# Performance work log

Measured on AMD Instinct MI355X. Metric: run time of the kernel, lower is better.

The kernel has to match this reference:

```python
import jax, jax.numpy as jnp
import numpy as np

NUM_HEADS = 16
N_EMBED = 1024
HEAD_SIZE = 64
BLOCK_SIZE = 2048


def setup_inputs() -> dict:
    key = jax.random.key(0)
    ks = jax.random.split(key, 6)
    B, S, C, H, D = 2, BLOCK_SIZE, N_EMBED, NUM_HEADS, HEAD_SIZE
    x = jax.random.normal(ks[0], (B, S, C), dtype=jnp.float32)
    scale = C ** -0.5
    # per-head q/k/v projections (bias=False), stacked over heads: [H, C, D]
    Wq = jax.random.normal(ks[1], (H, C, D), dtype=jnp.float32) * scale
    Wk = jax.random.normal(ks[2], (H, C, D), dtype=jnp.float32) * scale
    Wv = jax.random.normal(ks[3], (H, C, D), dtype=jnp.float32) * scale
    # output projection Linear(H*D, C)
    Wo = jax.random.normal(ks[4], (H * D, C), dtype=jnp.float32) * ((H * D) ** -0.5)
    bo = jax.random.normal(ks[5], (C,), dtype=jnp.float32) * 0.01
    return {"x": x, "Wq": Wq, "Wk": Wk, "Wv": Wv, "Wo": Wo, "bo": bo}


def reference(x, Wq, Wk, Wv, Wo, bo):
    B, S, C = x.shape
    H, _, D = Wq.shape
    # project: [B, H, S, D]
    q = jnp.einsum("bsc,hcd->bhsd", x, Wq)
    k = jnp.einsum("bsc,hcd->bhsd", x, Wk)
    v = jnp.einsum("bsc,hcd->bhsd", x, Wv)
    # scaled causal attention scores: [B, H, S, S]
    scores = jnp.einsum("bhsd,bhtd->bhst", q, k) * (D ** -0.5)
    causal = jnp.tril(jnp.ones((S, S), dtype=bool))
    scores = jnp.where(causal, scores, jnp.finfo(scores.dtype).min)
    attn = jax.nn.softmax(scores, axis=-1)
    out = jnp.einsum("bhst,bhtd->bhsd", attn, v)  # [B, H, S, D]
    # concat heads -> [B, S, H*D], then output projection
    out = out.transpose(0, 2, 1, 3).reshape(B, S, H * D)
    return out @ Wo + bo
```

## Files before the change

kernel.cpp:

```cpp
#include <hip/hip_runtime.h>
#include <cstdint>
#include <cstddef>

constexpr int SEQ  = 2048;
constexpr int CH   = 1024;
constexpr int NH   = 16;
constexpr int HS   = 64;
constexpr int NB   = 2;
constexpr int HDIM = NH * HS;

typedef __bf16 bf16x8 __attribute__((ext_vector_type(8)));
typedef __bf16 bf16x4 __attribute__((ext_vector_type(4)));
typedef float  f32x4  __attribute__((ext_vector_type(4)));

__device__ __forceinline__ unsigned short f2bf(float f) {
  union { float f; unsigned u; } v; v.f = f;
  unsigned u = v.u;
  u += 0x7fffu + ((u >> 16) & 1u);
  return (unsigned short)(u >> 16);
}
__device__ __forceinline__ float bf2f(unsigned short h) {
  union { unsigned u; float f; } v; v.u = ((unsigned)h) << 16;
  return v.f;
}
__device__ __forceinline__ float load_elem(const void* p, int flag, size_t idx) {
  if (flag) return ((const float*)p)[idx];
  return bf2f(((const unsigned short*)p)[idx]);
}
__device__ __forceinline__ void gl_lds16(const unsigned short* g, unsigned short* l) {
  __builtin_amdgcn_global_load_lds(
      (const __attribute__((address_space(1))) unsigned int*)g,
      (__attribute__((address_space(3))) unsigned int*)l, 16, 0, 0);
}

__device__ int detect_flag_block(const void* p, int n, int tid, int nthr) {
  __shared__ int det_good;
  if (tid == 0) det_good = 0;
  __syncthreads();
  const unsigned short* u = (const unsigned short*)p;
  int good = 0;
  for (int j = tid; j < n; j += nthr) {
    unsigned short v = u[2 * j];
    int e = (v >> 7) & 0xFF;
    if (v != 0 && e >= 90 && e <= 150) good++;
  }
  atomicAdd(&det_good, good);
  __syncthreads();
  return (det_good * 10 >= n * 7) ? 0 : 1;
}

__global__ __launch_bounds__(256) void prep(
    const void* __restrict__ x,  const void* __restrict__ wq,
    const void* __restrict__ wk, const void* __restrict__ wv,
    const void* __restrict__ wo,
    unsigned short* __restrict__ xb,
    unsigned short* __restrict__ wall,
    unsigned short* __restrict__ wot) {
  __shared__ unsigned short tile[32][36];
  int idx = blockIdx.x, tid = threadIdx.x;
  int row = tid >> 3, cg = (tid & 7) * 4;
  int col = tid >> 3, rg = (tid & 7) * 4;
  if (idx < 1024) {
    int f = detect_flag_block(x, 512, tid, 256);
    size_t n4 = (size_t)NB * SEQ * CH / 4;
    for (size_t i = (size_t)idx * 256 + tid; i < n4; i += (size_t)1024 * 256) {
      ushort4 o;
      if (f) {
        float4 v = ((const float4*)x)[i];
        o.x = f2bf(v.x); o.y = f2bf(v.y); o.z = f2bf(v.z); o.w = f2bf(v.w);
      } else {
        o = ((const ushort4*)x)[i];
      }
      ((ushort4*)xb)[i] = o;
    }
  } else if (idx < 4096) {
    int j = idx - 1024;
    int which = j >> 10, hh = (j >> 6) & 15, sub = j & 63;
    const void* src = (which == 0) ? wq : (which == 1) ? wk : wv;
    int f = detect_flag_block(src, 512, tid, 256);
    int c0 = (sub & 1) * 32;
    int r0 = (sub >> 1) * 32;
    size_t boff = (size_t)hh * CH * HS;
    size_t si = boff + (size_t)(r0 + row) * HS + c0 + cg;
    ushort4 t4;
    if (f) {
      float4 v = *(const float4*)((const float*)src + si);
      t4.x = f2bf(v.x); t4.y = f2bf(v.y); t4.z = f2bf(v.z); t4.w = f2bf(v.w);
    } else {
      t4 = *(const ushort4*)((const unsigned short*)src + si);
    }
    *(ushort4*)&tile[row][cg] = t4;
    __syncthreads();
    unsigned short* d = wall + ((size_t)which * NH + hh) * HS * CH;
    ushort4 o;
    o.x = tile[rg + 0][col]; o.y = tile[rg + 1][col];
    o.z = tile[rg + 2][col]; o.w = tile[rg + 3][col];
    *(ushort4*)&d[(size_t)(c0 + col) * CH + r0 + rg] = o;
  } else {
    int sub = idx - 4096;
    int f = detect_flag_block(wo, 512, tid, 256);
    int c0 = (sub & 31) * 32;
    int r0 = (sub >> 5) * 32;
    size_t si = (size_t)(r0 + row) * CH + c0 + cg;
    ushort4 t4;
    if (f) {
      float4 v = *(const float4*)((const float*)wo + si);
      t4.x = f2bf(v.x); t4.y = f2bf(v.y); t4.z = f2bf(v.z); t4.w = f2bf(v.w);
    } else {
      t4 = *(const ushort4*)((const unsigned short*)wo + si);
    }
    *(ushort4*)&tile[row][cg] = t4;
    __syncthreads();
    ushort4 o;
    o.x = tile[rg + 0][col]; o.y = tile[rg + 1][col];
    o.z = tile[rg + 2][col]; o.w = tile[rg + 3][col];
    *(ushort4*)&wot[(size_t)(c0 + col) * HDIM + r0 + rg] = o;
  }
}

__global__ __launch_bounds__(256, 2) void qkv_gemm(
    const unsigned short* __restrict__ xb,
    const unsigned short* __restrict__ wall,
    unsigned short* __restrict__ qo,
    unsigned short* __restrict__ ko,
    unsigned short* __restrict__ vt) {
  __shared__ __attribute__((aligned(16))) unsigned short Al[2][128 * 64];
  __shared__ __attribute__((aligned(16))) unsigned short Bl[2][192 * 64];
  int mt = blockIdx.x, nt = blockIdx.y;
  const unsigned short* A  = xb   + (size_t)mt * 128 * CH;
  const unsigned short* Bm = wall + (size_t)nt * 192 * CH;
  int tid = threadIdx.x, wave = tid >> 6, lane = tid & 63;
  int quad = lane >> 4, l15 = lane & 15;
  int r8 = lane >> 3, c8 = lane & 7;
  int gcol = ((c8 ^ r8) << 3);
  int x7 = l15 & 7;
  int wm = (wave >> 1) * 64, wn = (wave & 1) * 96;
  f32x4 acc[4][6];
  #pragma unroll
  for (int i = 0; i < 4; i++)
    #pragma unroll
    for (int j = 0; j < 6; j++) acc[i][j] = (f32x4){0.f, 0.f, 0.f, 0.f};

  auto stage = [&](int bb, int k0) {
    #pragma unroll
    for (int c = 0; c < 4; c++) {
      int row = wave * 32 + c * 8 + r8;
      gl_lds16(&A[(size_t)row * CH + k0 + gcol], &Al[bb][(wave * 32 + c * 8) * 64]);
    }
    #pragma unroll
    for (int c = 0; c < 6; c++) {
      int row = wave * 48 + c * 8 + r8;
      gl_lds16(&Bm[(size_t)row * CH + k0 + gcol], &Bl[bb][(wave * 48 + c * 8) * 64]);
    }
  };

  stage(0, 0);
  __syncthreads();
  for (int ks = 0; ks < 16; ks++) {
    int bb = ks & 1;
    if (ks < 15) stage(bb ^ 1, (ks + 1) * 64);
    #pragma unroll
    for (int h = 0; h < 2; h++) {
      int cq = ((quad + 4 * h) ^ x7) << 3;
      bf16x8 af[4], bfr[6];
      #pragma unroll
      for (int fm = 0; fm < 4; fm++)
        af[fm] = *reinterpret_cast<const bf16x8*>(&Al[bb][(wm + fm * 16 + l15) * 64 + cq]);
      #pragma unroll
      for (int fn = 0; fn < 6; fn++)
        bfr[fn] = *reinterpret_cast<const bf16x8*>(&Bl[bb][(wn + fn * 16 + l15) * 64 + cq]);
      __builtin_amdgcn_s_setprio(1);
      #pragma unroll
      for (int fm = 0; fm < 4; fm++)
        #pragma unroll
        for (int fn = 0; fn < 6; fn++)
          acc[fm][fn] = __builtin_amdgcn_mfma_f32_16x16x32_bf16(af[fm], bfr[fn], acc[fm][fn], 0, 0, 0);
      __builtin_amdgcn_s_setprio(0);
    }
    __syncthreads();
  }

  #pragma unroll
  for (int fn = 0; fn < 6; fn++) {
    int c0 = nt * 192 + wn + fn * 16;
    int seg = c0 >> 10;
    int hd = (c0 & 1023) + l15;
    int h = hd >> 6, d = hd & 63;
    if (seg < 2) {
      unsigned short* dst = (seg == 0) ? qo : ko;
      float s = (seg == 0) ? 0.18033688011112042f : 1.0f;
      #pragma unroll
      for (int fm = 0; fm < 4; fm++) {
        int m = mt * 128 + wm + fm * 16 + quad * 4;
        int b = m >> 11, s0 = m & 2047;
        #pragma unroll
        for (int r = 0; r < 4; r++)
          dst[(((size_t)b * NH + h) * SEQ + s0 + r) * HS + d] = f2bf(acc[fm][fn][r] * s);
      }
    } else {
      #pragma unroll
      for (int fm = 0; fm < 4; fm++) {
        int m = mt * 128 + wm + fm * 16 + quad * 4;
        int b = m >> 11, s0 = m & 2047;
        ushort4 pk;
        pk.x = f2bf(acc[fm][fn][0]); pk.y = f2bf(acc[fm][fn][1]);
        pk.z = f2bf(acc[fm][fn][2]); pk.w = f2bf(acc[fm][fn][3]);
        *(ushort4*)&vt[(((size_t)b * NH + h) * HS + d) * SEQ + s0] = pk;
      }
    }
  }
}

template <bool MASKED>
__device__ __forceinline__ void soft_pack(const f32x4* s, f32x4& ls,
                                          unsigned short* ptRow, int quad, int tmb) {
  #pragma unroll
  for (int tb = 0; tb < 4; tb++) {
    f32x4 pv;
    #pragma unroll
    for (int r = 0; r < 4; r++) {
      float p = __builtin_amdgcn_exp2f(s[tb][r]);
      if (MASKED) { if (tmb + tb * 16 + quad * 4 + r > 0) p = 0.f; }
      pv[r] = p;
    }
    ls += pv;
    bf16x4 pk;
    pk.x = (__bf16)pv[0]; pk.y = (__bf16)pv[1];
    pk.z = (__bf16)pv[2]; pk.w = (__bf16)pv[3];
    *(bf16x4*)&ptRow[tb * 16 + quad * 4] = pk;
  }
}

template <int QKM, bool PV0, bool PVV>
__device__ __forceinline__ void attn_step(
    const unsigned short (&Kb)[64][64], const unsigned short (&Vp)[64][64],
    unsigned short* p0row, unsigned short* p1row,
    const bf16x8 (&qf)[2][2], f32x4 (&lsum)[2], f32x4 (&accO)[2][4],
    int quad, int l15, int tmb) {
  constexpr bool C0 = (QKM <= 1);
  constexpr bool M0 = (QKM == 1);
  constexpr bool M1 = (QKM == 3);
  int x7 = l15 & 7;
  bf16x8 pb0[2], pb1[2];
  if (PVV) {
    #pragma unroll
    for (int tp = 0; tp < 2; tp++) {
      if (PV0) pb0[tp] = *reinterpret_cast<const bf16x8*>(&p0row[tp * 32 + quad * 8]);
      pb1[tp] = *reinterpret_cast<const bf16x8*>(&p1row[tp * 32 + quad * 8]);
    }
  }
  f32x4 s0[4], s1[4];
  #pragma unroll
  for (int tb = 0; tb < 4; tb++) { s0[tb] = (f32x4){0,0,0,0}; s1[tb] = (f32x4){0,0,0,0}; }
  __builtin_amdgcn_s_setprio(1);
  #pragma unroll
  for (int tb = 0; tb < 4; tb++)
    #pragma unroll
    for (int hh = 0; hh < 2; hh++) {
      bf16x8 kf = *reinterpret_cast<const bf16x8*>(
          &Kb[tb * 16 + l15][((hh * 4 + quad) ^ x7) << 3]);
      if (C0) s0[tb] = __builtin_amdgcn_mfma_f32_16x16x32_bf16(kf, qf[0][hh], s0[tb], 0, 0, 0);
      s1[tb] = __builtin_amdgcn_mfma_f32_16x16x32_bf16(kf, qf[1][hh], s1[tb], 0, 0, 0);
    }
  if (PVV) {
    #pragma unroll
    for (int db = 0; db < 4; db++)
      #pragma unroll
      for (int tp = 0; tp < 2; tp++) {
        bf16x8 vf = *reinterpret_cast<const bf16x8*>(
            &Vp[db * 16 + l15][((tp * 4 + quad) ^ x7) << 3]);
        if (PV0) accO[0][db] = __builtin_amdgcn_mfma_f32_16x16x32_bf16(vf, pb0[tp], accO[0][db], 0, 0, 0);
        accO[1][db] = __builtin_amdgcn_mfma_f32_16x16x32_bf16(vf, pb1[tp], accO[1][db], 0, 0, 0);
      }
  }
  __builtin_amdgcn_s_setprio(0);
  if (C0) soft_pack<M0>(s0, lsum[0], p0row, quad, tmb);
  soft_pack<M1>(s1, lsum[1], p1row, quad, tmb);
}

__global__ __launch_bounds__(256) void attn_k(
    const unsigned short* __restrict__ q,
    const unsigned short* __restrict__ k,
    const unsigned short* __restrict__ vt,
    unsigned short* __restrict__ y) {
  __shared__ __attribute__((aligned(16))) unsigned short Kl[3][64][64];
  __shared__ __attribute__((aligned(16))) unsigned short Vl[3][64][64];
  __shared__ __attribute__((aligned(16))) unsigned short Pt[4][16][152];

  int n = blockIdx.x + 16 * blockIdx.y;
  int g = n & 7, idx = n >> 3;
  int p = idx & 15;
  int bh = g * 4 + (idx >> 4);
  int st0 = p, st1 = 31 - p;
  int b = bh >> 4, h = bh & 15;
  const unsigned short* Q0 = q + ((size_t)bh * SEQ + st0 * 64) * HS;
  const unsigned short* Q1 = q + ((size_t)bh * SEQ + st1 * 64) * HS;
  const unsigned short* K  = k  + (size_t)bh * SEQ * HS;
  const unsigned short* V  = vt + (size_t)bh * HS * SEQ;
  int tid = threadIdx.x, wave = tid >> 6, lane = tid & 63;
  int quad = lane >> 4, l15 = lane & 15;
  int lr = tid >> 3, lc = (tid & 7) * 8;
  int sc = (((tid & 7) ^ (lr & 7)) << 3);

  bf16x8 qf[2][2];
  #pragma unroll
  for (int hh = 0; hh < 2; hh++) {
    qf[0][hh] = *reinterpret_cast<const bf16x8*>(
        &Q0[(size_t)(wave * 16 + l15) * HS + hh * 32 + quad * 8]);
    qf[1][hh] = *reinterpret_cast<const bf16x8*>(
        &Q1[(size_t)(wave * 16 + l15) * HS + hh * 32 + quad * 8]);
  }

  f32x4 lsum[2] = {(f32x4){0,0,0,0}, (f32x4){0,0,0,0}};
  f32x4 accO[2][4];
  #pragma unroll
  for (int f = 0; f < 2; f++)
    #pragma unroll
    for (int i = 0; i < 4; i++) accO[f][i] = (f32x4){0.f, 0.f, 0.f, 0.f};

  unsigned short* p0row = &Pt[wave][l15][0];
  unsigned short* p1row = &Pt[wave][l15][64];
  int tmb = -(wave * 16 + l15);

  const unsigned short* pK0 = K + (size_t)lr * HS + lc;
  const unsigned short* pK1 = pK0 + (size_t)32 * HS;
  const unsigned short* pV0 = V + (size_t)lr * SEQ + lc;
  const unsigned short* pV1 = pV0 + (size_t)32 * SEQ;
  uint4 kr0, kr1, vr0, vr1;
  auto g2r = [&]() {
    kr0 = *(const uint4*)pK0; kr1 = *(const uint4*)pK1;
    vr0 = *(const uint4*)pV0; vr1 = *(const uint4*)pV1;
    pK0 += 64 * HS; pK1 += 64 * HS; pV0 += 64; pV1 += 64;
  };
  auto r2l = [&](int nb) {
    *(uint4*)&Kl[nb][lr][sc] = kr0; *(uint4*)&Kl[nb][lr + 32][sc] = kr1;
    *(uint4*)&Vl[nb][lr][sc] = vr0; *(uint4*)&Vl[nb][lr + 32][sc] = vr1;
  };

  g2r(); r2l(0);
  __syncthreads();

  {
    if (st1 > 0) g2r();
    if (st0 == 0)
      attn_step<1, false, false>(Kl[0], Vl[2], p0row, p1row, qf, lsum, accO, quad, l15, tmb);
    else
      attn_step<0, false, false>(Kl[0], Vl[2], p0row, p1row, qf, lsum, accO, quad, l15, tmb);
    if (st1 > 0) r2l(1);
    __syncthreads();
  }
  for (int t = 1; t < st0; t++) {
    g2r();
    attn_step<0, true, true>(Kl[t % 3], Vl[(t + 2) % 3], p0row, p1row, qf, lsum, accO, quad, l15, tmb);
    r2l((t + 1) % 3);
    __syncthreads();
  }
  if (st0 >= 1) {
    int t = st0;
    g2r();
    attn_step<1, true, true>(Kl[t % 3], Vl[(t + 2) % 3], p0row, p1row, qf, lsum, accO, quad, l15, tmb);
    r2l((t + 1) % 3);
    __syncthreads();
  }
  {
    int t = st0 + 1;
    bool more = (t < st1);
    if (more) g2r();
    if (t == st1)
      attn_step<3, true, true>(Kl[t % 3], Vl[(t + 2) % 3], p0row, p1row, qf, lsum, accO, quad, l15, tmb);
    else
      attn_step<2, true, true>(Kl[t % 3], Vl[(t + 2) % 3], p0row, p1row, qf, lsum, accO, quad, l15, tmb);
    if (more) r2l((t + 1) % 3);
    __syncthreads();
  }
  for (int t = st0 + 2; t < st1; t++) {
    g2r();
    attn_step<2, false, true>(Kl[t % 3], Vl[(t + 2) % 3], p0row, p1row, qf, lsum, accO, quad, l15, tmb);
    r2l((t + 1) % 3);
    __syncthreads();
  }
  if (st1 >= st0 + 2) {
    int t = st1;
    attn_step<3, false, true>(Kl[t % 3], Vl[(t + 2) % 3], p0row, p1row, qf, lsum, accO, quad, l15, tmb);
  }
  {
    const unsigned short (&Vb)[64][64] = Vl[st1 % 3];
    int x7 = l15 & 7;
    bf16x8 pb1[2];
    #pragma unroll
    for (int tp = 0; tp < 2; tp++)
      pb1[tp] = *reinterpret_cast<const bf16x8*>(&p1row[tp * 32 + quad * 8]);
    #pragma unroll
    for (int db = 0; db < 4; db++)
      #pragma unroll
      for (int tp = 0; tp < 2; tp++) {
        bf16x8 vf = *reinterpret_cast<const bf16x8*>(
            &Vb[db * 16 + l15][((tp * 4 + quad) ^ x7) << 3]);
        accO[1][db] = __builtin_amdgcn_mfma_f32_16x16x32_bf16(vf, pb1[tp], accO[1][db], 0, 0, 0);
      }
  }

  #pragma unroll
  for (int f = 0; f < 2; f++) {
    float rs = (lsum[f][0] + lsum[f][1]) + (lsum[f][2] + lsum[f][3]);
    rs += __shfl_xor(rs, 16); rs += __shfl_xor(rs, 32);
    float inv = 1.0f / fmaxf(rs, 1e-30f);
    int srow = (f == 0 ? st0 : st1) * 64 + wave * 16 + l15;
    #pragma unroll
    for (int db = 0; db < 4; db++) {
      ushort4 pk;
      pk.x = f2bf(accO[f][db][0] * inv); pk.y = f2bf(accO[f][db][1] * inv);
      pk.z = f2bf(accO[f][db][2] * inv); pk.w = f2bf(accO[f][db][3] * inv);
      *(ushort4*)&y[((size_t)b * SEQ + srow) * HDIM + h * 64 + db * 16 + quad * 4] = pk;
    }
  }
}

__global__ __launch_bounds__(256) void out_gemm(
    const unsigned short* __restrict__ y,
    const unsigned short* __restrict__ wot,
    const void* __restrict__ bo,
    float* __restrict__ out) {
  __shared__ __attribute__((aligned(16))) unsigned short Al[2][128 * 64];
  __shared__ __attribute__((aligned(16))) unsigned short Bl[2][64 * 64];
  int tid = threadIdx.x;
  int fbo = detect_flag_block(bo, 512, tid, 256);
  int mt = blockIdx.x, nt = blockIdx.y;
  const unsigned short* A  = y   + (size_t)mt * 128 * HDIM;
  const unsigned short* Bm = wot + (size_t)nt * 64 * HDIM;
  int wave = tid >> 6, lane = tid & 63;
  int quad = lane >> 4, l15 = lane & 15;
  int r8 = lane >> 3, c8 = lane & 7;
  int gcol = ((c8 ^ r8) << 3);
  int x7 = l15 & 7;
  int wm = (wave >> 1) * 64, wn = (wave & 1) * 32;
  f32x4 acc[4][2];
  #pragma unroll
  for (int i = 0; i < 4; i++)
    #pragma unroll
    for (int j = 0; j < 2; j++) acc[i][j] = (f32x4){0.f, 0.f, 0.f, 0.f};

  auto stage = [&](int bb, int k0) {
    #pragma unroll
    for (int c = 0; c < 4; c++) {
      int row = wave * 32 + c * 8 + r8;
      gl_lds16(&A[(size_t)row * HDIM + k0 + gcol], &Al[bb][(wave * 32 + c * 8) * 64]);
    }
    #pragma unroll
    for (int c = 0; c < 2; c++) {
      int row = wave * 16 + c * 8 + r8;
      gl_lds16(&Bm[(size_t)row * HDIM + k0 + gcol], &Bl[bb][(wave * 16 + c * 8) * 64]);
    }
  };

  stage(0, 0);
  __syncthreads();
  for (int ks = 0; ks < 16; ks++) {
    int bb = ks & 1;
    if (ks < 15) stage(bb ^ 1, (ks + 1) * 64);
    #pragma unroll
    for (int h = 0; h < 2; h++) {
      int cq = ((quad + 4 * h) ^ x7) << 3;
      bf16x8 af[4], bfr[2];
      #pragma unroll
      for (int fm = 0; fm < 4; fm++)
        af[fm] = *reinterpret_cast<const bf16x8*>(&Al[bb][(wm + fm * 16 + l15) * 64 + cq]);
      #pragma unroll
      for (int fn = 0; fn < 2; fn++)
        bfr[fn] = *reinterpret_cast<const bf16x8*>(&Bl[bb][(wn + fn * 16 + l15) * 64 + cq]);
      __builtin_amdgcn_s_setprio(1);
      #pragma unroll
      for (int fm = 0; fm < 4; fm++)
        #pragma unroll
        for (int fn = 0; fn < 2; fn++)
          acc[fm][fn] = __builtin_amdgcn_mfma_f32_16x16x32_bf16(af[fm], bfr[fn], acc[fm][fn], 0, 0, 0);
      __builtin_amdgcn_s_setprio(0);
    }
    __syncthreads();
  }

  #pragma unroll
  for (int fn = 0; fn < 2; fn++) {
    int n = nt * 64 + wn + fn * 16 + l15;
    float bias = load_elem(bo, fbo, n);
    #pragma unroll
    for (int fm = 0; fm < 4; fm++) {
      int m = mt * 128 + wm + fm * 16 + quad * 4;
      #pragma unroll
      for (int r = 0; r < 4; r++)
        out[(size_t)(m + r) * CH + n] = acc[fm][fn][r] + bias;
    }
  }
}

extern "C" void kernel_launch(void* const* d_in, const int* in_sizes, int n_in,
                              void* d_out, int out_size, void* d_ws, size_t ws_size,
                              hipStream_t stream) {
  const void* x  = d_in[0];
  const void* Wq = d_in[1];
  const void* Wk = d_in[2];
  const void* Wv = d_in[3];
  const void* Wo = d_in[4];
  const void* bo = d_in[5];
  float* out = (float*)d_out;

  char* ws = (char*)d_ws;
  const size_t MB = 1024 * 1024;
  unsigned short* qb   = (unsigned short*)(ws + 0);
  unsigned short* kb   = (unsigned short*)(ws + 8  * MB);
  unsigned short* vtb  = (unsigned short*)(ws + 16 * MB);
  unsigned short* yb   = (unsigned short*)(ws + 24 * MB);
  unsigned short* wall = (unsigned short*)(ws + 32 * MB);
  unsigned short* wot  = (unsigned short*)(ws + 38 * MB);
  unsigned short* xb   = (unsigned short*)(ws + 40 * MB);

  prep<<<5120, 256, 0, stream>>>(x, Wq, Wk, Wv, Wo, xb, wall, wot);
  qkv_gemm<<<dim3(NB * SEQ / 128, 3 * HDIM / 192), 256, 0, stream>>>(xb, wall, qb, kb, vtb);
  attn_k<<<dim3(16, NB * NH), 256, 0, stream>>>(qb, kb, vtb, yb);
  out_gemm<<<dim3(NB * SEQ / 128, CH / 64), 256, 0, stream>>>(yb, wot, bo, out);
}
```

Baseline: 171.1 us.

## Fuse x fp32-to-bf16 conversion into QKV GEMM A-tile loading

The separate prep pass that converted x to bf16 in the workspace is removed. The QKV GEMM now loads fp32 x directly through registers, converts it, and writes the swizzled bf16 tile into LDS after the MFMA step, overlapping the load with compute. This saves a full write and read of the 8 MB bf16 x copy. The cost is that each GEMM block reads x as fp32, twice the bytes and repeated across the 16 N-tiles, uses more registers, and replaces async global-to-LDS copies with register staging.

```diff
diff --git a/kernel.cpp b/kernel.cpp
--- a/kernel.cpp
+++ b/kernel.cpp
@@ -50,32 +50,16 @@
 }
 
 __global__ __launch_bounds__(256) void prep(
-    const void* __restrict__ x,  const void* __restrict__ wq,
-    const void* __restrict__ wk, const void* __restrict__ wv,
-    const void* __restrict__ wo,
-    unsigned short* __restrict__ xb,
+    const void* __restrict__ wq, const void* __restrict__ wk,
+    const void* __restrict__ wv, const void* __restrict__ wo,
     unsigned short* __restrict__ wall,
     unsigned short* __restrict__ wot) {
   __shared__ unsigned short tile[32][36];
   int idx = blockIdx.x, tid = threadIdx.x;
   int row = tid >> 3, cg = (tid & 7) * 4;
   int col = tid >> 3, rg = (tid & 7) * 4;
-  if (idx < 1024) {
-    int f = detect_flag_block(x, 512, tid, 256);
-    size_t n4 = (size_t)NB * SEQ * CH / 4;
-    for (size_t i = (size_t)idx * 256 + tid; i < n4; i += (size_t)1024 * 256) {
-      ushort4 o;
-      if (f) {
-        float4 v = ((const float4*)x)[i];
-        o.x = f2bf(v.x); o.y = f2bf(v.y); o.z = f2bf(v.z); o.w = f2bf(v.w);
-      } else {
-        o = ((const ushort4*)x)[i];
-      }
-      ((ushort4*)xb)[i] = o;
-    }
-  } else if (idx < 4096) {
-    int j = idx - 1024;
-    int which = j >> 10, hh = (j >> 6) & 15, sub = j & 63;
+  if (idx < 3072) {
+    int which = idx >> 10, hh = (idx >> 6) & 15, sub = idx & 63;
     const void* src = (which == 0) ? wq : (which == 1) ? wk : wv;
     int f = detect_flag_block(src, 512, tid, 256);
     int c0 = (sub & 1) * 32;
@@ -97,7 +81,7 @@
     o.z = tile[rg + 2][col]; o.w = tile[rg + 3][col];
     *(ushort4*)&d[(size_t)(c0 + col) * CH + r0 + rg] = o;
   } else {
-    int sub = idx - 4096;
+    int sub = idx - 3072;
     int f = detect_flag_block(wo, 512, tid, 256);
     int c0 = (sub & 31) * 32;
     int r0 = (sub >> 5) * 32;
@@ -119,17 +103,17 @@
 }
 
 __global__ __launch_bounds__(256, 2) void qkv_gemm(
-    const unsigned short* __restrict__ xb,
+    const void* __restrict__ x,
     const unsigned short* __restrict__ wall,
     unsigned short* __restrict__ qo,
     unsigned short* __restrict__ ko,
     unsigned short* __restrict__ vt) {
   __shared__ __attribute__((aligned(16))) unsigned short Al[2][128 * 64];
   __shared__ __attribute__((aligned(16))) unsigned short Bl[2][192 * 64];
+  int tid = threadIdx.x, wave = tid >> 6, lane = tid & 63;
+  int fx = detect_flag_block(x, 512, tid, 256);
   int mt = blockIdx.x, nt = blockIdx.y;
-  const unsigned short* A  = xb   + (size_t)mt * 128 * CH;
   const unsigned short* Bm = wall + (size_t)nt * 192 * CH;
-  int tid = threadIdx.x, wave = tid >> 6, lane = tid & 63;
   int quad = lane >> 4, l15 = lane & 15;
   int r8 = lane >> 3, c8 = lane & 7;
   int gcol = ((c8 ^ r8) << 3);
@@ -141,12 +125,39 @@
     #pragma unroll
     for (int j = 0; j < 6; j++) acc[i][j] = (f32x4){0.f, 0.f, 0.f, 0.f};
 
-  auto stage = [&](int bb, int k0) {
+  const float*          xf = (const float*)x          + (size_t)mt * 128 * CH;
+  const unsigned short* xh = (const unsigned short*)x + (size_t)mt * 128 * CH;
+
+  float4 fa[4][2]; uint4 ua[4];
+  auto a_load = [&](int k0) {
     #pragma unroll
     for (int c = 0; c < 4; c++) {
-      int row = wave * 32 + c * 8 + r8;
-      gl_lds16(&A[(size_t)row * CH + k0 + gcol], &Al[bb][(wave * 32 + c * 8) * 64]);
-    }
+      size_t src = (size_t)(wave * 32 + c * 8 + r8) * CH + k0 + gcol;
+      if (fx) {
+        fa[c][0] = *(const float4*)(xf + src);
+        fa[c][1] = *(const float4*)(xf + src + 4);
+      } else {
+        ua[c] = *(const uint4*)(xh + src);
+      }
+    }
+  };
+  auto a_write = [&](int bb) {
+    #pragma unroll
+    for (int c = 0; c < 4; c++) {
+      unsigned short* d = &Al[bb][(wave * 32 + c * 8) * 64 + lane * 8];
+      if (fx) {
+        uint4 o;
+        o.x = (unsigned)f2bf(fa[c][0].x) | ((unsigned)f2bf(fa[c][0].y) << 16);
+        o.y = (unsigned)f2bf(fa[c][0].z) | ((unsigned)f2bf(fa[c][0].w) << 16);
+        o.z = (unsigned)f2bf(fa[c][1].x) | ((unsigned)f2bf(fa[c][1].y) << 16);
+        o.w = (unsigned)f2bf(fa[c][1].z) | ((unsigned)f2bf(fa[c][1].w) << 16);
+        *(uint4*)d = o;
+      } else {
+        *(uint4*)d = ua[c];
+      }
+    }
+  };
+  auto b_stage = [&](int bb, int k0) {
     #pragma unroll
     for (int c = 0; c < 6; c++) {
       int row = wave * 48 + c * 8 + r8;
@@ -154,11 +165,12 @@
     }
   };
 
-  stage(0, 0);
+  a_load(0); b_stage(0, 0);
+  a_write(0);
   __syncthreads();
   for (int ks = 0; ks < 16; ks++) {
     int bb = ks & 1;
-    if (ks < 15) stage(bb ^ 1, (ks + 1) * 64);
+    if (ks < 15) { a_load((ks + 1) * 64); b_stage(bb ^ 1, (ks + 1) * 64); }
     #pragma unroll
     for (int h = 0; h < 2; h++) {
       int cq = ((quad + 4 * h) ^ x7) << 3;
@@ -177,6 +189,7 @@
           acc[fm][fn] = __builtin_amdgcn_mfma_f32_16x16x32_bf16(af[fm], bfr[fn], acc[fm][fn], 0, 0, 0);
       __builtin_amdgcn_s_setprio(0);
     }
+    if (ks < 15) a_write(bb ^ 1);
     __syncthreads();
   }
 
@@ -512,10 +525,9 @@
   unsigned short* yb   = (unsigned short*)(ws + 24 * MB);
   unsigned short* wall = (unsigned short*)(ws + 32 * MB);
   unsigned short* wot  = (unsigned short*)(ws + 38 * MB);
-  unsigned short* xb   = (unsigned short*)(ws + 40 * MB);
-
-  prep<<<5120, 256, 0, stream>>>(x, Wq, Wk, Wv, Wo, xb, wall, wot);
-  qkv_gemm<<<dim3(NB * SEQ / 128, 3 * HDIM / 192), 256, 0, stream>>>(xb, wall, qb, kb, vtb);
+
+  prep<<<4096, 256, 0, stream>>>(Wq, Wk, Wv, Wo, wall, wot);
+  qkv_gemm<<<dim3(NB * SEQ / 128, 3 * HDIM / 192), 256, 0, stream>>>(x, wall, qb, kb, vtb);
   attn_k<<<dim3(16, NB * NH), 256, 0, stream>>>(qb, kb, vtb, yb);
   out_gemm<<<dim3(NB * SEQ / 128, CH / 64), 256, 0, stream>>>(yb, wot, bo, out);
 }
```

Result: slower. 252.9 us (+47.8%).
